# Kernel tuning notes

Measured on AMD Instinct MI355X. Metric: run time of the kernel, lower is better.

Reference implementation:

```python
import jax, jax.numpy as jnp
import numpy as np
from jax import lax


def conv2d(x, w, b, pad):
    # x: NCHW, w: OIHW
    out = lax.conv_general_dilated(x, w, (1, 1), [(pad, pad), (pad, pad)],
                                   dimension_numbers=('NCHW', 'OIHW', 'NCHW'))
    return out + b[None, :, None, None]


def traj_grid_sample(ps, gx, gy):
    """Faithful F.grid_sample (5D, trilinear, zeros padding, align_corners=False)
    applied to ps expanded along a depth axis of size L. Since every depth slice
    of the expanded input equals ps, we gather 2D from ps and fold the z-axis
    interpolation weights / bounds mask in analytically (no (B,C,L,H,W) expand).
    ps: (B,C,H,W); gx, gy: (B,L,H,W) pixel-coordinate flow fields."""
    B, C, H, W = ps.shape
    L = gx.shape[1]
    dt = ps.dtype
    # the original normalizes to [-1,1] assuming align_corners-style ranges
    gxn = gx / (W - 1) * 2 - 1
    gyn = gy / (H - 1) * 2 - 1
    gzn = jnp.arange(1, L + 1, dtype=dt) / (L - 1) * 2 - 1  # (L,)
    # torch grid_sample default align_corners=False unnormalization
    ix = ((gxn + 1) * W - 1) / 2
    iy = ((gyn + 1) * H - 1) / 2
    iz = jnp.broadcast_to((((gzn + 1) * L - 1) / 2)[None, :, None, None], ix.shape)
    x0 = jnp.floor(ix)
    y0 = jnp.floor(iy)
    z0 = jnp.floor(iz)
    bidx = jnp.arange(B)[:, None, None, None]
    out = jnp.zeros((B, L, H, W, C), dtype=dt)
    for dz in (0.0, 1.0):
        zc = z0 + dz
        wz = 1.0 - jnp.abs(iz - zc)
        mz = (zc >= 0) & (zc <= L - 1)
        for dy in (0.0, 1.0):
            yc = y0 + dy
            wy = 1.0 - jnp.abs(iy - yc)
            my = (yc >= 0) & (yc <= H - 1)
            yci = jnp.clip(yc, 0, H - 1).astype(jnp.int32)
            for dx in (0.0, 1.0):
                xc = x0 + dx
                wx = 1.0 - jnp.abs(ix - xc)
                mx = (xc >= 0) & (xc <= W - 1)
                xci = jnp.clip(xc, 0, W - 1).astype(jnp.int32)
                w = wz * wy * wx * (mz & my & mx).astype(dt)  # (B,L,H,W)
                val = ps[bidx, :, yci, xci]  # (B,L,H,W,C)
                out = out + val * w[..., None]
    return jnp.transpose(out, (0, 4, 1, 2, 3))  # (B,C,L,H,W)


def reference(x, prev_state, sub_w1, sub_b1, sub_w2, sub_b2,
              reset_w, reset_b, update_w, update_b, out_w, out_b,
              reset_ww, reset_wb, update_ww, update_wb, out_ww, out_wb):
    B, Ch, H, W = prev_state.shape
    L = sub_w2.shape[0] // 2
    # subCNN: flow generation
    s = jnp.concatenate([x, prev_state], axis=1)
    o = jax.nn.relu(conv2d(s, sub_w1, sub_b1, 2))
    o = jax.nn.relu(conv2d(o, sub_w2, sub_b2, 2))
    M = traj_grid_sample(prev_state, o[:, :L], o[:, L:])  # (B,Ch,L,H,W)
    Mf = M.reshape(B, Ch * L, H, W)  # view(B, C*L, H, W)
    update = jax.nn.sigmoid(conv2d(x, update_w, update_b, 1) + conv2d(Mf, update_ww, update_wb, 0))
    reset = jax.nn.sigmoid(conv2d(x, reset_w, reset_b, 1) + conv2d(Mf, reset_ww, reset_wb, 0))
    v = conv2d(x, out_w, out_b, 1) + reset * conv2d(Mf, out_ww, out_wb, 0)
    out_inputs = jnp.where(v >= 0, v, 0.2 * v)  # leaky_relu(0.2)
    return prev_state * update + out_inputs * (1.0 - update)


def setup_inputs() -> dict:
    key = jax.random.key(0)
    ks = jax.random.split(key, 12)
    B, Cin, Ch, L, H, W = 4, 8, 96, 13, 96, 96
    rn = lambda k, shape, s=0.05: jax.random.normal(k, shape, dtype=jnp.float32) * s
    z = lambda n: jnp.zeros((n,), jnp.float32)
    return {
        'x': rn(ks[0], (B, Cin, H, W), 1.0),
        'prev_state': rn(ks[1], (B, Ch, H, W), 1.0),
        'sub_w1': rn(ks[2], (32, Cin + Ch, 5, 5)), 'sub_b1': z(32),
        'sub_w2': rn(ks[3], (2 * L, 32, 5, 5)), 'sub_b2': z(2 * L),
        'reset_w': rn(ks[4], (Ch, Cin, 3, 3)), 'reset_b': z(Ch),
        'update_w': rn(ks[5], (Ch, Cin, 3, 3)), 'update_b': z(Ch),
        'out_w': rn(ks[6], (Ch, Cin, 3, 3)), 'out_b': z(Ch),
        'reset_ww': rn(ks[7], (Ch, Ch * L, 1, 1)), 'reset_wb': z(Ch),
        'update_ww': rn(ks[8], (Ch, Ch * L, 1, 1)), 'update_wb': z(Ch),
        'out_ww': rn(ks[9], (Ch, Ch * L, 1, 1)), 'out_wb': z(Ch),
    }
```

## Files before the change

### kernel.cpp

```cpp
#include <hip/hip_runtime.h>
#include <hip/hip_bf16.h>

#define HW 9216

typedef unsigned short ushort;
typedef unsigned int   uint;
typedef __attribute__((ext_vector_type(4))) float f32x4;
typedef __attribute__((ext_vector_type(2))) uint  u32x2;
typedef __attribute__((ext_vector_type(8))) short s16x8;

__device__ float  g_o1[4*32*HW];
__device__ float  g_q [2*4*26*HW];
__device__ __align__(16) float g_ht[4*HW*96];
__device__ __align__(16) ushort g_chi[4*(size_t)HW*128];
__device__ __align__(16) ushort g_clo[4*(size_t)HW*128];
__device__ __align__(16) ushort g_w1b[28*4*2048];
__device__ __align__(16) ushort g_a[36864*1248];
__device__ __align__(16) ushort g_b[18*39*512];
__device__ __align__(16) float  g_urv[2304*288*16];

__device__ __forceinline__ ushort f2b(float f){
  uint x = __float_as_uint(f);
  return (ushort)((x + 0x7FFFu + ((x >> 16) & 1u)) >> 16);
}
__device__ __forceinline__ float b2f(ushort h){
  return __uint_as_float(((uint)h) << 16);
}

__global__ void pack_b_k(const float* __restrict__ uww, const float* __restrict__ rww,
                         const float* __restrict__ vww){
  int i = blockIdx.x*256 + threadIdx.x;
  if (i >= 3*96*1248) return;
  int gate = i / (96*1248); int rem = i % (96*1248);
  int oc = rem / 1248;      int kp = rem % 1248;
  int l = kp / 96, c = kp % 96;
  const float* src = (gate == 0) ? uww : ((gate == 1) ? rww : vww);
  float v = src[oc*1248 + c*13 + l];
  int n  = gate*96 + oc;
  int nt = n >> 4, nl = n & 15;
  int kb = kp >> 5, kk = kp & 31;
  g_b[(nt*39 + kb)*512 + nl*32 + kk] = f2b(v);
}

__global__ void pack_w1b_k(const float* __restrict__ w1){
  int i = blockIdx.x*256 + threadIdx.x;
  if (i >= 25*4*1024) return;
  int tap = i >> 12;
  int cb  = (i >> 10) & 3;
  int oc  = (i >> 5) & 31;
  int kk  = i & 31;
  int ci  = cb*32 + kk;
  float w = (ci < 104) ? w1[oc*2600 + ci*25 + tap] : 0.f;
  ushort h = f2b(w);
  float rem = w - b2f(h);
  int base = ((tap*4 + cb) << 11) + (oc >> 4)*512 + (oc & 15)*32 + kk;
  g_w1b[base]        = h;
  g_w1b[base + 1024] = f2b(rem);
}

__global__ __launch_bounds__(256) void transpose_k(const float* __restrict__ hp,
                                                   const float* __restrict__ x){
  __shared__ float tile[32][33];
  int s0 = blockIdx.x*32;
  int b  = blockIdx.z;
  int t  = threadIdx.x;
  if (blockIdx.y < 3){
    int c0 = blockIdx.y*32;
    for (int i = t; i < 32*32; i += 256){
      int c = i >> 5, s = i & 31;
      tile[c][s] = hp[((size_t)(b*96 + c0 + c))*HW + s0 + s];
    }
    __syncthreads();
    for (int i = t; i < 32*32; i += 256){
      int s = i >> 5, c = i & 31;
      float v = tile[c][s];
      size_t px = (size_t)b*HW + s0 + s;
      g_ht[px*96 + c0 + c] = v;
      ushort h = f2b(v);
      g_chi[px*128 + 8 + c0 + c] = h;
      g_clo[px*128 + 8 + c0 + c] = f2b(v - b2f(h));
    }
  } else {
    for (int i = t; i < 8*32; i += 256){
      int c = i >> 5, s = i & 31;
      tile[c][s] = x[((size_t)(b*8 + c))*HW + s0 + s];
    }
    __syncthreads();
    for (int i = t; i < 32*8; i += 256){
      int s = i >> 3, c = i & 7;
      float v = tile[c][s];
      size_t px = (size_t)b*HW + s0 + s;
      ushort h = f2b(v);
      g_chi[px*128 + c] = h;
      g_clo[px*128 + c] = f2b(v - b2f(h));
    }
  }
}

__global__ __launch_bounds__(256) void conv1_mfma_k(const float* __restrict__ b1){
  __shared__ __align__(16) ushort sh[2*160*128];
  int t = threadIdx.x;
  int w = t >> 6, lane = t & 63;
  int nl = lane & 15, q = lane >> 4;
  int rt = blockIdx.x / 6, ct = blockIdx.x % 6;
  int b  = blockIdx.z;
  int r0 = rt*4, c0 = ct*16;
  const size_t pbase = (size_t)b*HW;

  #pragma unroll
  for (int i = 0; i < 20; i++){
    int idx = i*256 + t;
    int half = (i >= 10) ? 1 : 0;
    int rem = idx - half*2560;
    int px = rem >> 4, ci = rem & 15;
    int cs = ci ^ (px & 15);
    int r = px / 20, c = px - r*20;
    int gr = r0 + r - 2, gc = c0 + c - 2;
    f32x4 v = (f32x4){0.f,0.f,0.f,0.f};
    if ((unsigned)gr < 96u && (unsigned)gc < 96u){
      const ushort* src = half ? g_clo : g_chi;
      v = *(const f32x4*)(src + ((pbase + (size_t)(gr*96 + gc)) << 7) + cs*8);
    }
    *(f32x4*)((char*)sh + (size_t)idx*16) = v;
  }
  __syncthreads();

  int kxA[7], kyA[7], tpA[7];
  #pragma unroll
  for (int i = 0; i < 7; i++){
    int tp  = 7*w + i;
    int tpc = (tp > 24) ? 24 : tp;
    kyA[i] = tpc / 5;
    kxA[i] = tpc - kyA[i]*5;
    tpA[i] = tp;
  }
  int foff = nl*32 + q*8;

  f32x4 acc[4][2];
  #pragma unroll
  for (int mr = 0; mr < 4; mr++){
    acc[mr][0] = (f32x4){0.f,0.f,0.f,0.f};
    acc[mr][1] = (f32x4){0.f,0.f,0.f,0.f};
  }

  for (int cb = 0; cb < 4; cb++){
    const ushort* bpc = g_w1b + ((size_t)cb << 11);
    s16x8 bq[3][4];
#define LOADB(slot, i) { const ushort* bp = bpc + ((size_t)tpA[i] << 13); \
    bq[slot][0] = *(const s16x8*)(bp + foff); \
    bq[slot][1] = *(const s16x8*)(bp + 512 + foff); \
    bq[slot][2] = *(const s16x8*)(bp + 1024 + foff); \
    bq[slot][3] = *(const s16x8*)(bp + 1536 + foff); }
    LOADB(0, 0); LOADB(1, 1);

    #pragma unroll
    for (int i = 0; i < 7; i++){
      if (i < 5) LOADB((i + 2) % 3, i + 2);
      int ky = kyA[i], kx = kxA[i];
      int chq = cb*4 + q;
      s16x8 ah[4], al[4];
      #pragma unroll
      for (int mr = 0; mr < 4; mr++){
        int px  = (mr + ky)*20 + kx + nl;
        int off = px*256 + (((chq ^ (px & 15))) << 4);
        ah[mr] = *(const s16x8*)((const char*)sh + off);
        al[mr] = *(const s16x8*)((const char*)sh + 40960 + off);
      }
      const int cur = i % 3;
      #pragma unroll
      for (int mr = 0; mr < 4; mr++){
        acc[mr][0] = __builtin_amdgcn_mfma_f32_16x16x32_bf16(ah[mr], bq[cur][0], acc[mr][0], 0,0,0);
        acc[mr][1] = __builtin_amdgcn_mfma_f32_16x16x32_bf16(ah[mr], bq[cur][1], acc[mr][1], 0,0,0);
      }
      #pragma unroll
      for (int mr = 0; mr < 4; mr++){
        acc[mr][0] = __builtin_amdgcn_mfma_f32_16x16x32_bf16(al[mr], bq[cur][0], acc[mr][0], 0,0,0);
        acc[mr][1] = __builtin_amdgcn_mfma_f32_16x16x32_bf16(al[mr], bq[cur][1], acc[mr][1], 0,0,0);
      }
      #pragma unroll
      for (int mr = 0; mr < 4; mr++){
        acc[mr][0] = __builtin_amdgcn_mfma_f32_16x16x32_bf16(ah[mr], bq[cur][2], acc[mr][0], 0,0,0);
        acc[mr][1] = __builtin_amdgcn_mfma_f32_16x16x32_bf16(ah[mr], bq[cur][3], acc[mr][1], 0,0,0);
      }
    }
#undef LOADB
  }

  __syncthreads();
  float* red = (float*)sh;
  #pragma unroll
  for (int mr = 0; mr < 4; mr++)
    #pragma unroll
    for (int nt = 0; nt < 2; nt++)
      *(f32x4*)&red[(((mr*2 + nt)*4 + w) << 8) + lane*4] = acc[mr][nt];
  __syncthreads();

  int mr = w;
  #pragma unroll
  for (int nt = 0; nt < 2; nt++){
    f32x4 s = (f32x4){0.f,0.f,0.f,0.f};
    #pragma unroll
    for (int ww = 0; ww < 4; ww++)
      s += *(f32x4*)&red[(((mr*2 + nt)*4 + ww) << 8) + lane*4];
    int oc = nt*16 + nl;
    float bias = b1[oc];
    s.x = fmaxf(s.x + bias, 0.f); s.y = fmaxf(s.y + bias, 0.f);
    s.z = fmaxf(s.z + bias, 0.f); s.w = fmaxf(s.w + bias, 0.f);
    *(f32x4*)(g_o1 + ((size_t)(b*32 + oc))*HW + (size_t)(r0 + mr)*96 + c0 + q*4) = s;
  }
}

__global__ __launch_bounds__(256) void conv2_k(const float* __restrict__ wt2,
                                               const float* __restrict__ b2){
  __shared__ __align__(16) float in_sh[8][20][24];
  __shared__ __align__(16) float w_sh[8][25][32];
  int tile = blockIdx.x;
  int kg   = blockIdx.y;
  int b    = blockIdx.z;
  int row0 = (tile / 6) * 16, col0 = (tile % 6) * 16;
  int t = threadIdx.x;
  int og  = t >> 5;
  int pos = t & 31;
  int row = pos >> 1, x0 = (pos & 1)*8;

  float acc[8][4];
  #pragma unroll
  for (int j = 0; j < 8; j++)
    #pragma unroll
    for (int o = 0; o < 4; o++) acc[j][o] = 0.f;

  for (int cc = 0; cc < 2; cc++){
    __syncthreads();
    for (int idx = t; idx < 8*20*24; idx += 256){
      int i = idx / 480, rem = idx % 480;
      int r = rem / 24, c = rem % 24;
      int gr = row0 + r - 2, gc = col0 + c - 2;
      float v = 0.f;
      if ((unsigned)gr < 96u && (unsigned)gc < 96u){
        int ci = kg*16 + cc*8 + i;
        v = g_o1[(b*32 + ci)*HW + gr*96 + gc];
      }
      in_sh[i][r][c] = v;
    }
    for (int idx = t; idx < 8*25*32; idx += 256){
      int i = idx / 800, rem = idx % 800;
      int tap = rem / 32, oc = rem % 32;
      int ci = kg*16 + cc*8 + i;
      w_sh[i][tap][oc] = (oc < 26) ? wt2[oc*800 + ci*25 + tap] : 0.f;
    }
    __syncthreads();

    for (int i = 0; i < 8; i++){
      #pragma unroll
      for (int ky = 0; ky < 5; ky++){
        const float* rp = &in_sh[i][row + ky][x0];
        f32x4 s0 = *(const f32x4*)(rp);
        f32x4 s1 = *(const f32x4*)(rp + 4);
        f32x4 s2 = *(const f32x4*)(rp + 8);
        float seg[12] = {s0.x,s0.y,s0.z,s0.w, s1.x,s1.y,s1.z,s1.w, s2.x,s2.y,s2.z,s2.w};
        #pragma unroll
        for (int kx = 0; kx < 5; kx++){
          f32x4 wv = *(const f32x4*)&w_sh[i][ky*5 + kx][og*4];
          #pragma unroll
          for (int j = 0; j < 8; j++){
            float a = seg[kx + j];
            acc[j][0] += a*wv.x; acc[j][1] += a*wv.y;
            acc[j][2] += a*wv.z; acc[j][3] += a*wv.w;
          }
        }
      }
    }
  }

  int rg = row0 + row, cg = col0 + x0;
  #pragma unroll
  for (int o = 0; o < 4; o++){
    int slot = og*4 + o;
    if (slot < 26){
      float bias = (kg == 0) ? b2[slot] : 0.f;
      float* d = g_q + (size_t)kg*4*26*HW + ((size_t)(b*26 + slot))*HW + rg*96 + cg;
      #pragma unroll
      for (int j = 0; j < 8; j++) d[j] = acc[j][o] + bias;
    }
  }
}

__global__ __launch_bounds__(384) void sample_k(){
  __shared__ float cw[13][4][16];
  __shared__ int   co[13][4][16];
  int pt = blockIdx.x;
  int t  = threadIdx.x;
  int b  = pt / 576;
  int p0 = (pt % 576) * 16;

  if (t < 208){
    int m = t/13, l = t%13;
    int p = p0 + m;
    const int NQ = 4*26*HW;
    float gx = fmaxf(g_q[(b*26 + l     )*HW + p] + g_q[NQ + (b*26 + l     )*HW + p], 0.f);
    float gy = fmaxf(g_q[(b*26 + 13 + l)*HW + p] + g_q[NQ + (b*26 + 13 + l)*HW + p], 0.f);
    float ix = gx * (96.f/95.f) - 0.5f;
    float iy = gy * (96.f/95.f) - 0.5f;
    float iz = (float)(l+1) * (13.f/12.f) - 0.5f;
    float z0 = floorf(iz);
    float zf = 0.f;
    #pragma unroll
    for (int dz = 0; dz < 2; dz++){
      float zc = z0 + (float)dz;
      float wz = 1.f - fabsf(iz - zc);
      if (zc >= 0.f && zc <= 12.f) zf += wz;
    }
    float x0f = floorf(ix), y0f = floorf(iy);
    #pragma unroll
    for (int dy = 0; dy < 2; dy++){
      float yc = y0f + (float)dy;
      float wy = 1.f - fabsf(iy - yc);
      bool  my = (yc >= 0.f) && (yc <= 95.f);
      int  yci = min(max((int)yc, 0), 95);
      #pragma unroll
      for (int dx = 0; dx < 2; dx++){
        float xc = x0f + (float)dx;
        float wx = 1.f - fabsf(ix - xc);
        bool  mx = (xc >= 0.f) && (xc <= 95.f);
        int  xci = min(max((int)xc, 0), 95);
        cw[l][dy*2+dx][m] = (mx && my) ? zf*wy*wx : 0.f;
        co[l][dy*2+dx][m] = yci*96 + xci;
      }
    }
  }
  __syncthreads();

  int m  = t & 15;
  int cq = t >> 4;
  int c0 = cq*4;
  const float* hb = g_ht + (size_t)b*HW*96 + c0;
  int kb3 = cq >> 3;
  int kk  = (cq & 7)*4;
  for (int l = 0; l < 13; l++){
    float w0 = cw[l][0][m], w1 = cw[l][1][m], w2 = cw[l][2][m], w3 = cw[l][3][m];
    int   o0 = co[l][0][m], o1 = co[l][1][m], o2 = co[l][2][m], o3 = co[l][3][m];
    f32x4 v0 = *(const f32x4*)(hb + (size_t)o0*96);
    f32x4 v1 = *(const f32x4*)(hb + (size_t)o1*96);
    f32x4 v2 = *(const f32x4*)(hb + (size_t)o2*96);
    f32x4 v3 = *(const f32x4*)(hb + (size_t)o3*96);
    f32x4 acc = w0*v0 + w1*v1 + w2*v2 + w3*v3;
    int kb = l*3 + kb3;
    u32x2 pk;
    pk.x = (uint)f2b(acc.x) | ((uint)f2b(acc.y) << 16);
    pk.y = (uint)f2b(acc.z) | ((uint)f2b(acc.w) << 16);
    *(u32x2*)&g_a[(size_t)(pt*39 + kb)*512 + m*32 + kk] = pk;
  }
}

__global__ __launch_bounds__(256) void gemm_k(){
  __shared__ __align__(16) ushort Bsh[18*512];
  int w    = threadIdx.x >> 6;
  int lane = threadIdx.x & 63;
  int pt   = blockIdx.x*4 + w;
  int nl   = lane & 15, quad = lane >> 4;
  int t    = threadIdx.x;

  f32x4 acc[18];
  #pragma unroll
  for (int nt = 0; nt < 18; nt++) acc[nt] = (f32x4){0.f,0.f,0.f,0.f};

  const s16x8* Ab = reinterpret_cast<const s16x8*>(g_a);
  const uint*  Bg = reinterpret_cast<const uint*>(g_b);
  uint* Bs32 = (uint*)Bsh;
  int foff = nl*4 + quad;

  for (int kb = 0; kb < 39; kb++){
    __syncthreads();
    #pragma unroll
    for (int u = 0; u < 18; u++){
      int idx = u*256 + t;
      Bs32[idx] = Bg[(idx >> 8)*39*256 + kb*256 + (idx & 255)];
    }
    __syncthreads();
    s16x8 a = Ab[(pt*39 + kb)*64 + foff];
    #pragma unroll
    for (int nt = 0; nt < 18; nt++){
      s16x8 bf = *(const s16x8*)&Bsh[nt*512 + nl*32 + quad*8];
      acc[nt] = __builtin_amdgcn_mfma_f32_16x16x32_bf16(a, bf, acc[nt], 0, 0, 0);
    }
  }

  float* dst = g_urv + (size_t)pt*4608;
  #pragma unroll
  for (int nt = 0; nt < 18; nt++)
    *(f32x4*)&dst[(nt*16 + nl)*16 + quad*4] = acc[nt];
}

__global__ __launch_bounds__(256) void gate_k(const float* __restrict__ x,
                        const float* __restrict__ hp,
                        const float* __restrict__ uw, const float* __restrict__ ub,
                        const float* __restrict__ rw, const float* __restrict__ rb,
                        const float* __restrict__ vw, const float* __restrict__ vb,
                        const float* __restrict__ uwb, const float* __restrict__ rwb,
                        const float* __restrict__ vwb, float* __restrict__ out){
  int p  = blockIdx.x*256 + threadIdx.x;
  int oc = blockIdx.y;
  int b  = blockIdx.z;
  int h = p/96, w = p%96;
  float xU = ub[oc], xR = rb[oc], xV = vb[oc];
  const float* xb = x + b*8*HW;
  for (int ky = 0; ky < 3; ky++){
    int r = h+ky-1;
    if ((unsigned)r >= 96u) continue;
    for (int kx = 0; kx < 3; kx++){
      int c = w+kx-1;
      if ((unsigned)c >= 96u) continue;
      int off = r*96 + c;
      int wo  = ky*3 + kx;
      #pragma unroll
      for (int ic = 0; ic < 8; ic++){
        float a = xb[ic*HW + off];
        xU += a * uw[oc*72 + ic*9 + wo];
        xR += a * rw[oc*72 + ic*9 + wo];
        xV += a * vw[oc*72 + ic*9 + wo];
      }
    }
  }
  int pt = b*576 + (p >> 4), px = p & 15;
  const float* ur = g_urv + (size_t)pt*4608 + px;
  float gU = ur[(0*96 + oc)*16] + uwb[oc];
  float gR = ur[(1*96 + oc)*16] + rwb[oc];
  float gV = ur[(2*96 + oc)*16] + vwb[oc];
  float u = 1.f / (1.f + __expf(-(xU + gU)));
  float r = 1.f / (1.f + __expf(-(xR + gR)));
  float v = xV + r * gV;
  float oi = (v >= 0.f) ? v : 0.2f*v;
  float h0 = hp[(b*96 + oc)*HW + p];
  out[(b*96 + oc)*HW + p] = h0*u + oi*(1.f - u);
}

extern "C" void kernel_launch(void* const* d_in, const int* in_sizes, int n_in,
                              void* d_out, int out_size, void* d_ws, size_t ws_size,
                              hipStream_t stream){
  const float* x    = (const float*)d_in[0];
  const float* hp   = (const float*)d_in[1];
  const float* sw1  = (const float*)d_in[2];
  const float* sb1  = (const float*)d_in[3];
  const float* sw2  = (const float*)d_in[4];
  const float* sb2  = (const float*)d_in[5];
  const float* rw   = (const float*)d_in[6];
  const float* rb   = (const float*)d_in[7];
  const float* uw   = (const float*)d_in[8];
  const float* ub   = (const float*)d_in[9];
  const float* vw   = (const float*)d_in[10];
  const float* vb   = (const float*)d_in[11];
  const float* rww  = (const float*)d_in[12];
  const float* rwb  = (const float*)d_in[13];
  const float* uww  = (const float*)d_in[14];
  const float* uwb  = (const float*)d_in[15];
  const float* vww  = (const float*)d_in[16];
  const float* vwb  = (const float*)d_in[17];

  pack_b_k    <<<dim3((3*96*1248 + 255)/256), dim3(256), 0, stream>>>(uww, rww, vww);
  pack_w1b_k  <<<dim3((25*4*1024 + 255)/256), dim3(256), 0, stream>>>(sw1);
  transpose_k <<<dim3(288, 4, 4), dim3(256), 0, stream>>>(hp, x);
  conv1_mfma_k<<<dim3(144, 1, 4), dim3(256), 0, stream>>>(sb1);
  conv2_k     <<<dim3(36, 2, 4), dim3(256), 0, stream>>>(sw2, sb2);
  sample_k    <<<dim3(2304),     dim3(384), 0, stream>>>();
  gemm_k      <<<dim3(576),      dim3(256), 0, stream>>>();
  gate_k      <<<dim3(36, 96, 4), dim3(256), 0, stream>>>(x, hp,
               uw, ub, rw, rb, vw, vb, uwb, rwb, vwb, (float*)d_out);
}
```

Measured before the change: 404.1 us.

## Fuse trajectory grid sampling into the MFMA GEMM, dropping the bf16 A buffer

The separate sampling kernel, which wrote a large bf16 A matrix (about 92 MB) to global memory, is removed. The GEMM kernel now computes bilinear weights and offsets for its 64 points into shared memory, then gathers from the transposed hidden state and builds each MFMA A fragment in registers. This removes the write and re-read of the intermediate and one launch. In exchange the GEMM does scattered gathers inside its k-loop, which may add latency between the barriers, and it uses more shared memory.

```diff
diff --git a/kernel.cpp b/kernel.cpp
--- a/kernel.cpp
+++ b/kernel.cpp
@@ -6,7 +6,8 @@
 typedef unsigned short ushort;
 typedef unsigned int   uint;
 typedef __attribute__((ext_vector_type(4))) float f32x4;
-typedef __attribute__((ext_vector_type(2))) uint  u32x2;
+typedef __attribute__((ext_vector_type(4))) uint  u32x4;
+typedef __attribute__((ext_vector_type(4))) int   i32x4;
 typedef __attribute__((ext_vector_type(8))) short s16x8;
 
 __device__ float  g_o1[4*32*HW];
@@ -15,7 +16,6 @@
 __device__ __align__(16) ushort g_chi[4*(size_t)HW*128];
 __device__ __align__(16) ushort g_clo[4*(size_t)HW*128];
 __device__ __align__(16) ushort g_w1b[28*4*2048];
-__device__ __align__(16) ushort g_a[36864*1248];
 __device__ __align__(16) ushort g_b[18*39*512];
 __device__ __align__(16) float  g_urv[2304*288*16];
 
@@ -285,18 +285,22 @@
   }
 }
 
-__global__ __launch_bounds__(384) void sample_k(){
-  __shared__ float cw[13][4][16];
-  __shared__ int   co[13][4][16];
-  int pt = blockIdx.x;
-  int t  = threadIdx.x;
-  int b  = pt / 576;
-  int p0 = (pt % 576) * 16;
-
-  if (t < 208){
-    int m = t/13, l = t%13;
-    int p = p0 + m;
-    const int NQ = 4*26*HW;
+__global__ __launch_bounds__(256) void gemm_k(){
+  __shared__ __align__(16) ushort Bsh[18*512];
+  __shared__ __align__(16) float cw4[13][64][4];
+  __shared__ __align__(16) int   co4[13][64][4];
+  int t = threadIdx.x;
+  int w = t >> 6, lane = t & 63;
+  int nl = lane & 15, quad = lane >> 4;
+  int blk = blockIdx.x;
+  int b   = blk / 144;
+  int pbase0 = (blk % 144) * 64;
+  int pt  = blk*4 + w;
+
+  const int NQ = 4*26*HW;
+  for (int idx = t; idx < 832; idx += 256){
+    int l = idx >> 6, m = idx & 63;
+    int p = pbase0 + m;
     float gx = fmaxf(g_q[(b*26 + l     )*HW + p] + g_q[NQ + (b*26 + l     )*HW + p], 0.f);
     float gy = fmaxf(g_q[(b*26 + 13 + l)*HW + p] + g_q[NQ + (b*26 + 13 + l)*HW + p], 0.f);
     float ix = gx * (96.f/95.f) - 0.5f;
@@ -323,66 +327,55 @@
         float wx = 1.f - fabsf(ix - xc);
         bool  mx = (xc >= 0.f) && (xc <= 95.f);
         int  xci = min(max((int)xc, 0), 95);
-        cw[l][dy*2+dx][m] = (mx && my) ? zf*wy*wx : 0.f;
-        co[l][dy*2+dx][m] = yci*96 + xci;
-      }
-    }
-  }
-  __syncthreads();
-
-  int m  = t & 15;
-  int cq = t >> 4;
-  int c0 = cq*4;
-  const float* hb = g_ht + (size_t)b*HW*96 + c0;
-  int kb3 = cq >> 3;
-  int kk  = (cq & 7)*4;
-  for (int l = 0; l < 13; l++){
-    float w0 = cw[l][0][m], w1 = cw[l][1][m], w2 = cw[l][2][m], w3 = cw[l][3][m];
-    int   o0 = co[l][0][m], o1 = co[l][1][m], o2 = co[l][2][m], o3 = co[l][3][m];
-    f32x4 v0 = *(const f32x4*)(hb + (size_t)o0*96);
-    f32x4 v1 = *(const f32x4*)(hb + (size_t)o1*96);
-    f32x4 v2 = *(const f32x4*)(hb + (size_t)o2*96);
-    f32x4 v3 = *(const f32x4*)(hb + (size_t)o3*96);
-    f32x4 acc = w0*v0 + w1*v1 + w2*v2 + w3*v3;
-    int kb = l*3 + kb3;
-    u32x2 pk;
-    pk.x = (uint)f2b(acc.x) | ((uint)f2b(acc.y) << 16);
-    pk.y = (uint)f2b(acc.z) | ((uint)f2b(acc.w) << 16);
-    *(u32x2*)&g_a[(size_t)(pt*39 + kb)*512 + m*32 + kk] = pk;
-  }
-}
-
-__global__ __launch_bounds__(256) void gemm_k(){
-  __shared__ __align__(16) ushort Bsh[18*512];
-  int w    = threadIdx.x >> 6;
-  int lane = threadIdx.x & 63;
-  int pt   = blockIdx.x*4 + w;
-  int nl   = lane & 15, quad = lane >> 4;
-  int t    = threadIdx.x;
+        cw4[l][m][dy*2+dx] = (mx && my) ? zf*wy*wx : 0.f;
+        co4[l][m][dy*2+dx] = yci*96 + xci;
+      }
+    }
+  }
 
   f32x4 acc[18];
   #pragma unroll
   for (int nt = 0; nt < 18; nt++) acc[nt] = (f32x4){0.f,0.f,0.f,0.f};
 
-  const s16x8* Ab = reinterpret_cast<const s16x8*>(g_a);
-  const uint*  Bg = reinterpret_cast<const uint*>(g_b);
+  const uint* Bg = reinterpret_cast<const uint*>(g_b);
   uint* Bs32 = (uint*)Bsh;
-  int foff = nl*4 + quad;
-
+  const float* hb = g_ht + (size_t)b*HW*96 + quad*8;
+  int mloc = w*16 + nl;
+
+  int l = 0, kb3 = 0;
   for (int kb = 0; kb < 39; kb++){
     __syncthreads();
+    f32x4 wv = *(const f32x4*)cw4[l][mloc];
+    i32x4 ov = *(const i32x4*)co4[l][mloc];
+    const float* hc = hb + kb3*32;
+    const float* p0 = hc + (size_t)ov.x*96;
+    const float* p1 = hc + (size_t)ov.y*96;
+    const float* p2 = hc + (size_t)ov.z*96;
+    const float* p3 = hc + (size_t)ov.w*96;
+    f32x4 v0a = *(const f32x4*)(p0), v0b = *(const f32x4*)(p0 + 4);
+    f32x4 v1a = *(const f32x4*)(p1), v1b = *(const f32x4*)(p1 + 4);
+    f32x4 v2a = *(const f32x4*)(p2), v2b = *(const f32x4*)(p2 + 4);
+    f32x4 v3a = *(const f32x4*)(p3), v3b = *(const f32x4*)(p3 + 4);
     #pragma unroll
     for (int u = 0; u < 18; u++){
       int idx = u*256 + t;
       Bs32[idx] = Bg[(idx >> 8)*39*256 + kb*256 + (idx & 255)];
     }
     __syncthreads();
-    s16x8 a = Ab[(pt*39 + kb)*64 + foff];
+    f32x4 aA = wv.x*v0a + wv.y*v1a + wv.z*v2a + wv.w*v3a;
+    f32x4 aB = wv.x*v0b + wv.y*v1b + wv.z*v2b + wv.w*v3b;
+    union { u32x4 u; s16x8 s; } cv;
+    cv.u.x = (uint)f2b(aA.x) | ((uint)f2b(aA.y) << 16);
+    cv.u.y = (uint)f2b(aA.z) | ((uint)f2b(aA.w) << 16);
+    cv.u.z = (uint)f2b(aB.x) | ((uint)f2b(aB.y) << 16);
+    cv.u.w = (uint)f2b(aB.z) | ((uint)f2b(aB.w) << 16);
+    s16x8 a = cv.s;
     #pragma unroll
     for (int nt = 0; nt < 18; nt++){
       s16x8 bf = *(const s16x8*)&Bsh[nt*512 + nl*32 + quad*8];
       acc[nt] = __builtin_amdgcn_mfma_f32_16x16x32_bf16(a, bf, acc[nt], 0, 0, 0);
     }
+    kb3++; if (kb3 == 3){ kb3 = 0; l++; }
   }
 
   float* dst = g_urv + (size_t)pt*4608;
@@ -461,7 +454,6 @@
   transpose_k <<<dim3(288, 4, 4), dim3(256), 0, stream>>>(hp, x);
   conv1_mfma_k<<<dim3(144, 1, 4), dim3(256), 0, stream>>>(sb1);
   conv2_k     <<<dim3(36, 2, 4), dim3(256), 0, stream>>>(sw2, sb2);
-  sample_k    <<<dim3(2304),     dim3(384), 0, stream>>>();
   gemm_k      <<<dim3(576),      dim3(256), 0, stream>>>();
   gate_k      <<<dim3(36, 96, 4), dim3(256), 0, stream>>>(x, hp,
                uw, ub, rw, rb, vw, vb, uwb, rwb, vwb, (float*)d_out);
```

Result: faster. 389.1 us (-3.7%).
